# Performance work log

Measured on AMD Instinct MI355X. Metric: run time of the kernel, lower is better.

The kernel has to match this reference:

```python
import jax, jax.numpy as jnp
import numpy as np

B, T, D, H, C = 128, 1000, 40, 128, 8  # batch, time, input feats, hidden, classes


def _lstm_layer(x, Wih, Whh, bih, bhh):
    """Unidirectional LSTM over time. x: [B,T,Din] -> [B,T,H]. PyTorch gate order i,f,g,o."""
    Bn = x.shape[0]
    Hn = Whh.shape[1]
    b = bih + bhh
    def step(carry, xt):
        h, c = carry
        g = xt @ Wih.T + h @ Whh.T + b  # [B,4H]
        i, f, gg, o = jnp.split(g, 4, axis=-1)
        c = jax.nn.sigmoid(f) * c + jax.nn.sigmoid(i) * jnp.tanh(gg)
        h = jax.nn.sigmoid(o) * jnp.tanh(c)
        return (h, c), h
    h0 = jnp.zeros((Bn, Hn), x.dtype)
    _, hs = jax.lax.scan(step, (h0, h0), jnp.swapaxes(x, 0, 1))  # scan over time
    return jnp.swapaxes(hs, 0, 1)


def _bilstm_layer(x, pf, pb):
    fwd = _lstm_layer(x, *pf)
    bwd = jnp.flip(_lstm_layer(jnp.flip(x, 1), *pb), 1)
    return jnp.concatenate([fwd, bwd], axis=-1)  # [B,T,2H]


def setup_inputs() -> dict:
    key = jax.random.key(0)
    ks = jax.random.split(key, 16)
    s = 0.05
    def rn(k, shape):
        return jax.random.normal(k, shape, jnp.float32) * s
    inp = {"x": jax.random.normal(ks[0], (B, T, D), jnp.float32)}
    inp["ln_g"] = jnp.ones((D,), jnp.float32)
    inp["ln_b"] = jnp.zeros((D,), jnp.float32)
    dims = [D, 2 * H]  # layer-0 input feats, layer-1 input feats
    i = 1
    for l in range(2):
        for d in ("f", "b"):
            inp[f"Wih_{d}{l}"] = rn(ks[i], (4 * H, dims[l])); i += 1
            inp[f"Whh_{d}{l}"] = rn(ks[i], (4 * H, H)); i += 1
            inp[f"bih_{d}{l}"] = jnp.zeros((4 * H,), jnp.float32)
            inp[f"bhh_{d}{l}"] = jnp.zeros((4 * H,), jnp.float32)
    inp["attn_W1"] = rn(ks[i], (H, 2 * H)); i += 1
    inp["attn_b1"] = jnp.zeros((H,), jnp.float32)
    inp["attn_w2"] = rn(ks[i], (1, H)); i += 1
    inp["fc_W1"] = rn(ks[i], (H, 2 * H)); i += 1
    inp["fc_b1"] = jnp.zeros((H,), jnp.float32)
    inp["fc_W2"] = rn(ks[i], (C, H)); i += 1
    inp["fc_b2"] = jnp.zeros((C,), jnp.float32)
    return inp


def reference(x, ln_g, ln_b,
              Wih_f0, Whh_f0, bih_f0, bhh_f0, Wih_b0, Whh_b0, bih_b0, bhh_b0,
              Wih_f1, Whh_f1, bih_f1, bhh_f1, Wih_b1, Whh_b1, bih_b1, bhh_b1,
              attn_W1, attn_b1, attn_w2, fc_W1, fc_b1, fc_W2, fc_b2):
    # LayerNorm over feature dim (eps=1e-5, PyTorch default)
    mu = jnp.mean(x, axis=-1, keepdims=True)
    var = jnp.var(x, axis=-1, keepdims=True)
    xn = (x - mu) * jax.lax.rsqrt(var + 1e-5) * ln_g + ln_b
    # 2-layer bidirectional LSTM
    h = _bilstm_layer(xn, (Wih_f0, Whh_f0, bih_f0, bhh_f0), (Wih_b0, Whh_b0, bih_b0, bhh_b0))
    h = _bilstm_layer(h, (Wih_f1, Whh_f1, bih_f1, bhh_f1), (Wih_b1, Whh_b1, bih_b1, bhh_b1))
    # attention pooling: Linear-Tanh-Linear(no bias) -> softmax over time
    scores = jnp.tanh(h @ attn_W1.T + attn_b1) @ attn_w2[0]  # [B,T]
    w = jax.nn.softmax(scores, axis=1)
    ctx = jnp.einsum('bt,btd->bd', w, h)  # [B,2H]
    # MLP classifier head
    hid = jax.nn.relu(ctx @ fc_W1.T + fc_b1)
    return hid @ fc_W2.T + fc_b2  # [B,C] logits
```

## Files before the change

### kernel.cpp

```cpp
#include <hip/hip_runtime.h>

#define T_ 1000

__device__ __forceinline__ float sigf(float x) { return 1.0f / (1.0f + __expf(-x)); }
__device__ __forceinline__ float tanh_fast(float x) { return 1.0f - 2.0f / (1.0f + __expf(2.0f * x)); }
__device__ __forceinline__ float dot4(float4 a, float4 b) {
  return a.x * b.x + a.y * b.y + a.z * b.z + a.w * b.w;
}
__device__ __forceinline__ unsigned short f2bf(float f) {
  unsigned u = __float_as_uint(f);
  u = (u + 0x7fffu + ((u >> 16) & 1u)) >> 16;
  return (unsigned short)u;
}
__device__ __forceinline__ float bf2f(unsigned short h) {
  return __uint_as_float(((unsigned)h) << 16);
}
__device__ __forceinline__ float4 bf4_to_f4(ushort4 u) {
  float4 r;
  r.x = bf2f(u.x); r.y = bf2f(u.y); r.z = bf2f(u.z); r.w = bf2f(u.w);
  return r;
}

__global__ void bail_kernel(float* out, int n) {
  for (int i = threadIdx.x; i < n; i += 256) out[i] = 0.0f;
}

__global__ __launch_bounds__(256) void ln_stats_kernel(const float* __restrict__ x,
                                                       float* __restrict__ mu_arr,
                                                       float* __restrict__ rs_arr) {
  const int lane = threadIdx.x & 63;
  const int w = threadIdx.x >> 6;
  const long row = (long)blockIdx.x * 4 + w;
  float v = (lane < 40) ? x[row * 40 + lane] : 0.0f;
  float s1 = v, s2 = v * v;
  for (int m = 32; m; m >>= 1) {
    s1 += __shfl_xor(s1, m, 64);
    s2 += __shfl_xor(s2, m, 64);
  }
  if (lane == 0) {
    const float mu = s1 * (1.0f / 40.0f);
    const float var = s2 * (1.0f / 40.0f) - mu * mu;
    mu_arr[row] = mu;
    rs_arr[row] = rsqrtf(var + 1e-5f);
  }
}

__global__ __launch_bounds__(512, 1) void rec0_kernel(
    const float* __restrict__ x,
    const float* __restrict__ mu_arr, const float* __restrict__ rs_arr,
    const float* __restrict__ ln_g, const float* __restrict__ ln_b,
    const float* __restrict__ Wih_f, const float* __restrict__ Whh_f,
    const float* __restrict__ bih_f, const float* __restrict__ bhh_f,
    const float* __restrict__ Wih_b, const float* __restrict__ Whh_b,
    const float* __restrict__ bih_b, const float* __restrict__ bhh_b,
    float* __restrict__ h0) {
  const int tid = threadIdx.x;
  const int u = (tid >> 6) * 16 + ((tid & 63) >> 2);
  const int p = tid & 3;
  const int brow = blockIdx.x & 127;
  const int dir = blockIdx.x >> 7;
  const float* __restrict__ Wih = dir ? Wih_b : Wih_f;
  const float* __restrict__ Whh = dir ? Whh_b : Whh_f;
  const float* __restrict__ bih = dir ? bih_b : bih_f;
  const float* __restrict__ bhh = dir ? bhh_b : bhh_f;

  float4 wh[4][8];
  float4 wi[4][3];
  float S1[4], bias[4];
#pragma unroll
  for (int g = 0; g < 4; ++g) {
    const int row = g * 128 + u;
    const float4* wr = (const float4*)(Whh + row * 128 + p * 32);
#pragma unroll
    for (int ff = 0; ff < 8; ++ff) wh[g][ff] = wr[(ff + 2 * p) & 7];
    float s1p = 0.0f, s2p = 0.0f;
#pragma unroll
    for (int f = 0; f < 3; ++f) {
      float tmp[4];
#pragma unroll
      for (int e = 0; e < 4; ++e) {
        const int k = p * 12 + f * 4 + e;
        const float wv = (k < 40) ? Wih[row * 40 + k] : 0.0f;
        const float gk = (k < 40) ? ln_g[k] : 0.0f;
        const float bk = (k < 40) ? ln_b[k] : 0.0f;
        const float wf = wv * gk;
        tmp[e] = wf;
        s1p += wf;
        s2p += wv * bk;
      }
      wi[g][f] = make_float4(tmp[0], tmp[1], tmp[2], tmp[3]);
    }
    s1p += __shfl_xor(s1p, 1, 64); s1p += __shfl_xor(s1p, 2, 64);
    s2p += __shfl_xor(s2p, 1, 64); s2p += __shfl_xor(s2p, 2, 64);
    S1[g] = s1p;
    bias[g] = bih[g * 128 + u] + bhh[g * 128 + u] + s2p;
  }

  __shared__ float h4f[128];
  __shared__ __align__(16) float x_ring[2][8][48];
  __shared__ float mu_ring[2][8], rs_ring[2][8];
  __shared__ float hring[2][8][128];

  const int lr8 = tid / 40;
  const int lcol = tid - lr8 * 40;
  const long xbase = (long)brow * T_ * 40;
  const long mbase = (long)brow * T_;
  const long hbase = (long)brow * T_ * 256;

  if (tid < 128) h4f[tid] = 0.0f;
  if (tid < 128) {
    const int b = tid >> 6, r = (tid >> 3) & 7, cc = 40 + (tid & 7);
    x_ring[b][r][cc] = 0.0f;
  }
  if (tid < 320) {
    const int t = lr8;
    const int tt = dir ? (T_ - 1 - t) : t;
    x_ring[0][lr8][lcol] = x[xbase + (long)tt * 40 + lcol];
  } else if (tid < 328) {
    const int t = tid - 320;
    const int tt = dir ? (T_ - 1 - t) : t;
    mu_ring[0][t] = mu_arr[mbase + tt];
  } else if (tid < 336) {
    const int t = tid - 328;
    const int tt = dir ? (T_ - 1 - t) : t;
    rs_ring[0][t] = rs_arr[mbase + tt];
  }
  float c = 0.0f;
  float xpf = 0.0f, mupf = 0.0f, rspf = 0.0f;
  __syncthreads();

  for (int sb = 0; sb < 125; ++sb) {
    const int rb = sb & 1;
#pragma unroll
    for (int su = 0; su < 8; ++su) {
      if (su == 0) {
        if (sb + 1 < 125) {
          if (tid < 320) {
            const int t = (sb + 1) * 8 + lr8;
            const int tt = dir ? (T_ - 1 - t) : t;
            xpf = x[xbase + (long)tt * 40 + lcol];
          } else if (tid < 328) {
            const int t = (sb + 1) * 8 + (tid - 320);
            const int tt = dir ? (T_ - 1 - t) : t;
            mupf = mu_arr[mbase + tt];
          } else if (tid < 336) {
            const int t = (sb + 1) * 8 + (tid - 328);
            const int tt = dir ? (T_ - 1 - t) : t;
            rspf = rs_arr[mbase + tt];
          }
        }
        if (sb > 0) {
#pragma unroll
          for (int e = 0; e < 2; ++e) {
            const int idx = tid + e * 512;
            const int v = idx >> 7, j = idx & 127;
            const int ts = (sb - 1) * 8 + v;
            const int te = dir ? (T_ - 1 - ts) : ts;
            h0[hbase + (long)te * 256 + dir * 128 + j] = hring[rb ^ 1][v][j];
          }
        }
      }
      float a0 = 0.f, a1 = 0.f, a2 = 0.f, a3 = 0.f;
      const float4* h4v = (const float4*)h4f;
#pragma unroll
      for (int ff = 0; ff < 8; ++ff) {
        const float4 hv = h4v[p * 8 + ((ff + 2 * p) & 7)];
        a0 += dot4(hv, wh[0][ff]);
        a1 += dot4(hv, wh[1][ff]);
        a2 += dot4(hv, wh[2][ff]);
        a3 += dot4(hv, wh[3][ff]);
      }
      float x0 = 0.f, x1 = 0.f, x2 = 0.f, x3 = 0.f;
      const float4* xr4 = (const float4*)x_ring[rb][su];
#pragma unroll
      for (int f = 0; f < 3; ++f) {
        const float4 xv = xr4[p * 3 + f];
        x0 += dot4(xv, wi[0][f]);
        x1 += dot4(xv, wi[1][f]);
        x2 += dot4(xv, wi[2][f]);
        x3 += dot4(xv, wi[3][f]);
      }
      const float rs = rs_ring[rb][su];
      const float mu = mu_ring[rb][su];
      float pg[4];
      pg[0] = a0 + rs * x0;
      pg[1] = a1 + rs * x1;
      pg[2] = a2 + rs * x2;
      pg[3] = a3 + rs * x3;
#pragma unroll
      for (int g = 0; g < 4; ++g) {
        pg[g] += __shfl_xor(pg[g], 1, 64);
        pg[g] += __shfl_xor(pg[g], 2, 64);
        pg[g] += bias[g] - rs * mu * S1[g];
      }
      const float ig = sigf(pg[0]);
      const float fg = sigf(pg[1]);
      const float gg = tanh_fast(pg[2]);
      const float og = sigf(pg[3]);
      c = fg * c + ig * gg;
      const float hv = og * tanh_fast(c);
      if (p == 0) { h4f[u] = hv; hring[rb][su][u] = hv; }
      if (su == 7 && sb + 1 < 125) {
        if (tid < 320) x_ring[rb ^ 1][lr8][lcol] = xpf;
        else if (tid < 328) mu_ring[rb ^ 1][tid - 320] = mupf;
        else if (tid < 336) rs_ring[rb ^ 1][tid - 328] = rspf;
      }
      __syncthreads();
    }
  }
#pragma unroll
  for (int e = 0; e < 2; ++e) {
    const int idx = tid + e * 512;
    const int v = idx >> 7, j = idx & 127;
    const int ts = 124 * 8 + v;
    const int te = dir ? (T_ - 1 - ts) : ts;
    h0[hbase + (long)te * 256 + dir * 128 + j] = hring[0][v][j];
  }
}

__global__ __launch_bounds__(512, 1) void rec1_kernel(
    const float* __restrict__ xw_f, const float* __restrict__ xw_b,
    const float* __restrict__ Whh_f, const float* __restrict__ bih_f, const float* __restrict__ bhh_f,
    const float* __restrict__ Whh_b, const float* __restrict__ bih_b, const float* __restrict__ bhh_b,
    unsigned short* __restrict__ h1b, float* __restrict__ state,
    int Tc, int t0f, int t0b, int first) {
  const int tid = threadIdx.x;
  const int u = (tid >> 6) * 16 + ((tid & 63) >> 2);
  const int p = tid & 3;
  const int brow = blockIdx.x & 127;
  const int dir = blockIdx.x >> 7;
  const float* __restrict__ xw = dir ? xw_b : xw_f;
  const float* __restrict__ Whh = dir ? Whh_b : Whh_f;
  const float* __restrict__ bih = dir ? bih_b : bih_f;
  const float* __restrict__ bhh = dir ? bhh_b : bhh_f;
  const int t0 = dir ? t0b : t0f;

  float4 wh[4][8];
#pragma unroll
  for (int g = 0; g < 4; ++g) {
    const float4* wr = (const float4*)(Whh + (g * 128 + u) * 128 + p * 32);
#pragma unroll
    for (int ff = 0; ff < 8; ++ff) wh[g][ff] = wr[(ff + 2 * p) & 7];
  }
  const int myrow = p * 128 + u;
  const float bias_p = bih[myrow] + bhh[myrow];

  __shared__ float h4f[128];
  __shared__ float hring[2][8][128];
  float* sblk = state + (long)blockIdx.x * 256;
  float c = 0.0f;
  if (first) {
    if (tid < 128) h4f[tid] = 0.0f;
  } else {
    if (tid < 128) h4f[tid] = sblk[tid];
    c = sblk[128 + u];
  }
  const long gbase = (long)brow * Tc;
  float xr[8];
#pragma unroll
  for (int v = 0; v < 8; ++v) {
    xr[v] = 0.0f;
    if (v < Tc) {
      const int tr = dir ? (Tc - 1 - v) : v;
      xr[v] = xw[(gbase + tr) * 512 + myrow];
    }
  }
  __syncthreads();

  const int nSB = (Tc + 7) / 8;
  for (int sb = 0; sb < nSB; ++sb) {
    const int rb = sb & 1;
#pragma unroll
    for (int su = 0; su < 8; ++su) {
      const int s = sb * 8 + su;
      if (s >= Tc) break;
      if (su == 0 && sb > 0) {
#pragma unroll
        for (int e = 0; e < 2; ++e) {
          const int idx = tid + e * 512;
          const int v = idx >> 7, j = idx & 127;
          const int s2 = (sb - 1) * 8 + v;
          const int tt = dir ? (Tc - 1 - s2) : s2;
          h1b[((long)brow * T_ + (t0 + tt)) * 256 + dir * 128 + j] = f2bf(hring[rb ^ 1][v][j]);
        }
      }
      float a0 = 0.f, a1 = 0.f, a2 = 0.f, a3 = 0.f;
      const float4* h4v = (const float4*)h4f;
#pragma unroll
      for (int ff = 0; ff < 8; ++ff) {
        const float4 hv = h4v[p * 8 + ((ff + 2 * p) & 7)];
        a0 += dot4(hv, wh[0][ff]);
        a1 += dot4(hv, wh[1][ff]);
        a2 += dot4(hv, wh[2][ff]);
        a3 += dot4(hv, wh[3][ff]);
      }
      const float xin = xr[su] + bias_p;
      float pg[4];
      pg[0] = a0 + ((p == 0) ? xin : 0.0f);
      pg[1] = a1 + ((p == 1) ? xin : 0.0f);
      pg[2] = a2 + ((p == 2) ? xin : 0.0f);
      pg[3] = a3 + ((p == 3) ? xin : 0.0f);
#pragma unroll
      for (int g = 0; g < 4; ++g) {
        pg[g] += __shfl_xor(pg[g], 1, 64);
        pg[g] += __shfl_xor(pg[g], 2, 64);
      }
      const float ig = sigf(pg[0]);
      const float fg = sigf(pg[1]);
      const float gg = tanh_fast(pg[2]);
      const float og = sigf(pg[3]);
      c = fg * c + ig * gg;
      const float hv = og * tanh_fast(c);
      if (p == 0) { h4f[u] = hv; hring[rb][su][u] = hv; }
      if (su == 7) {
#pragma unroll
        for (int v = 0; v < 8; ++v) {
          const int sn = s + 1 + v;
          xr[v] = 0.0f;
          if (sn < Tc) {
            const int tr = dir ? (Tc - 1 - sn) : sn;
            xr[v] = xw[(gbase + tr) * 512 + myrow];
          }
        }
      }
      __syncthreads();
    }
  }
  {
    const int sbL = (Tc - 1) >> 3;
    const int cnt = Tc - sbL * 8;
    const int rbL = sbL & 1;
#pragma unroll
    for (int e = 0; e < 2; ++e) {
      const int idx = tid + e * 512;
      const int v = idx >> 7, j = idx & 127;
      if (v < cnt) {
        const int s2 = sbL * 8 + v;
        const int tt = dir ? (Tc - 1 - s2) : s2;
        h1b[((long)brow * T_ + (t0 + tt)) * 256 + dir * 128 + j] = f2bf(hring[rbL][v][j]);
      }
    }
  }
  if (tid < 128) sblk[tid] = h4f[tid];
  if (p == 0) sblk[128 + u] = c;
}

__global__ __launch_bounds__(256, 2) void gemm_xw1(
    const float* __restrict__ h0,
    const float* __restrict__ Wf, const float* __restrict__ Wb,
    float* __restrict__ xwf, float* __restrict__ xwb,
    int Tc, int t0f, int t0b) {
  __shared__ float As[64 * 36];
  __shared__ float Bs[128 * 36];
  __shared__ int rowbase[64];
  const int tid = threadIdx.x;
  const int tx = tid & 15, ty = tid >> 4;
  const int r0 = blockIdx.x * 64;
  const int jt = blockIdx.y;
  const int dir = jt >> 2;
  const int nh = jt & 3;
  const float* __restrict__ W = dir ? Wb : Wf;
  float* __restrict__ out = dir ? xwb : xwf;
  const int jbase = nh * 128;
  const int t0 = dir ? t0b : t0f;

  if (tid < 64) {
    const int r = r0 + tid;
    const int br = r / Tc;
    rowbase[tid] = br * T_ + t0 + (r - br * Tc);
  }

  float4* As4 = (float4*)As;
  float4* Bs4 = (float4*)Bs;
  float acc[4][8] = {};
#pragma unroll 1
  for (int kk = 0; kk < 8; ++kk) {
    __syncthreads();
#pragma unroll
    for (int i = 0; i < 2; ++i) {
      const int q = tid + i * 256;
      const int row = q >> 3, k4 = q & 7;
      As4[row * 9 + k4] = *(const float4*)&h0[(long)rowbase[row] * 256 + kk * 32 + k4 * 4];
    }
#pragma unroll
    for (int i = 0; i < 4; ++i) {
      const int q = tid + i * 256;
      const int row = q >> 3, k4 = q & 7;
      Bs4[row * 9 + k4] = *(const float4*)&W[(long)(jbase + row) * 256 + kk * 32 + k4 * 4];
    }
    __syncthreads();
#pragma unroll 1
    for (int k4 = 0; k4 < 8; ++k4) {
      float4 av[4];
#pragma unroll
      for (int r = 0; r < 4; ++r) av[r] = As4[(ty * 4 + r) * 9 + k4];
#pragma unroll
      for (int c2 = 0; c2 < 8; ++c2) {
        const float4 bv = Bs4[(tx + 16 * c2) * 9 + k4];
#pragma unroll
        for (int r = 0; r < 4; ++r) acc[r][c2] += dot4(av[r], bv);
      }
    }
  }
#pragma unroll
  for (int r = 0; r < 4; ++r) {
    const long ob = (long)(r0 + ty * 4 + r) * 512 + jbase + tx;
#pragma unroll
    for (int c2 = 0; c2 < 8; ++c2) out[ob + c2 * 16] = acc[r][c2];
  }
}

__global__ __launch_bounds__(256, 2) void score_kernel(
    const unsigned short* __restrict__ h1b, const float* __restrict__ W1,
    const float* __restrict__ b1, const float* __restrict__ w2,
    float* __restrict__ scores) {
  __shared__ float As[64 * 36];
  __shared__ float Bs[128 * 36];
  const int tid = threadIdx.x;
  const int tx = tid & 15, ty = tid >> 4;
  const long r0 = (long)blockIdx.x * 64;

  float4* As4 = (float4*)As;
  float4* Bs4 = (float4*)Bs;
  float acc[4][8] = {};
#pragma unroll 1
  for (int kk = 0; kk < 8; ++kk) {
    __syncthreads();
#pragma unroll
    for (int i = 0; i < 2; ++i) {
      const int q = tid + i * 256;
      const int row = q >> 3, k4 = q & 7;
      const ushort4 uv = *(const ushort4*)&h1b[(r0 + row) * 256 + kk * 32 + k4 * 4];
      As4[row * 9 + k4] = bf4_to_f4(uv);
    }
#pragma unroll
    for (int i = 0; i < 4; ++i) {
      const int q = tid + i * 256;
      const int row = q >> 3, k4 = q & 7;
      Bs4[row * 9 + k4] = *(const float4*)&W1[(long)row * 256 + kk * 32 + k4 * 4];
    }
    __syncthreads();
#pragma unroll 1
    for (int k4 = 0; k4 < 8; ++k4) {
      float4 av[4];
#pragma unroll
      for (int r = 0; r < 4; ++r) av[r] = As4[(ty * 4 + r) * 9 + k4];
#pragma unroll
      for (int c2 = 0; c2 < 8; ++c2) {
        const float4 bv = Bs4[(tx + 16 * c2) * 9 + k4];
#pragma unroll
        for (int r = 0; r < 4; ++r) acc[r][c2] += dot4(av[r], bv);
      }
    }
  }
#pragma unroll
  for (int r = 0; r < 4; ++r) {
    float s = 0.0f;
#pragma unroll
    for (int c2 = 0; c2 < 8; ++c2) {
      const int col = tx + 16 * c2;
      s += tanh_fast(acc[r][c2] + b1[col]) * w2[col];
    }
#pragma unroll
    for (int m = 1; m < 16; m <<= 1) s += __shfl_xor(s, m, 16);
    if (tx == 0) scores[r0 + ty * 4 + r] = s;
  }
}

__global__ __launch_bounds__(256, 2) void head_kernel(
    const float* __restrict__ scores, const unsigned short* __restrict__ h1b,
    const float* __restrict__ fW1, const float* __restrict__ fb1,
    const float* __restrict__ fW2, const float* __restrict__ fb2,
    float* __restrict__ outp) {
  const int b = blockIdx.x, tid = threadIdx.x;
  __shared__ float wls[1000];
  __shared__ float red[8];
  __shared__ __align__(16) float ctx[256];
  __shared__ __align__(16) float hid[128];

  float sv[4];
  float mx = -1e30f;
#pragma unroll
  for (int i = 0; i < 4; ++i) {
    const int t = tid + i * 256;
    sv[i] = (t < 1000) ? scores[b * 1000 + t] : -1e30f;
    mx = fmaxf(mx, sv[i]);
  }
  for (int m = 32; m; m >>= 1) mx = fmaxf(mx, __shfl_xor(mx, m, 64));
  if ((tid & 63) == 0) red[tid >> 6] = mx;
  __syncthreads();
  mx = fmaxf(fmaxf(red[0], red[1]), fmaxf(red[2], red[3]));
  float se = 0.0f;
#pragma unroll
  for (int i = 0; i < 4; ++i) {
    const int t = tid + i * 256;
    if (t < 1000) {
      const float e = __expf(sv[i] - mx);
      wls[t] = e;
      se += e;
    }
  }
  for (int m = 32; m; m >>= 1) se += __shfl_xor(se, m, 64);
  if ((tid & 63) == 0) red[4 + (tid >> 6)] = se;
  __syncthreads();
  const float rinv = 1.0f / (red[4] + red[5] + red[6] + red[7]);

  float a = 0.0f;
  const unsigned short* hb = h1b + (long)b * T_ * 256 + tid;
  for (int t = 0; t < T_; ++t) a = fmaf(wls[t], bf2f(hb[t * 256]), a);
  ctx[tid] = a * rinv;
  __syncthreads();
  if (tid < 128) {
    float s = fb1[tid];
    const float4* wr = (const float4*)&fW1[tid * 256];
    const float4* cc = (const float4*)ctx;
#pragma unroll
    for (int f = 0; f < 64; ++f) s += dot4(wr[f], cc[f]);
    hid[tid] = fmaxf(s, 0.0f);
  }
  __syncthreads();
  if (tid < 8) {
    float s = fb2[tid];
    const float4* wr = (const float4*)&fW2[tid * 128];
    const float4* hh = (const float4*)hid;
#pragma unroll
    for (int f = 0; f < 32; ++f) s += dot4(wr[f], hh[f]);
    outp[b * 8 + tid] = s;
  }
}

extern "C" void kernel_launch(void* const* d_in, const int* in_sizes, int n_in,
                              void* d_out, int out_size, void* d_ws, size_t ws_size,
                              hipStream_t stream) {
  (void)in_sizes; (void)n_in; (void)out_size;
  const float* x       = (const float*)d_in[0];
  const float* ln_g    = (const float*)d_in[1];
  const float* ln_b    = (const float*)d_in[2];
  const float* Wih_f0  = (const float*)d_in[3];
  const float* Whh_f0  = (const float*)d_in[4];
  const float* bih_f0  = (const float*)d_in[5];
  const float* bhh_f0  = (const float*)d_in[6];
  const float* Wih_b0  = (const float*)d_in[7];
  const float* Whh_b0  = (const float*)d_in[8];
  const float* bih_b0  = (const float*)d_in[9];
  const float* bhh_b0  = (const float*)d_in[10];
  const float* Wih_f1  = (const float*)d_in[11];
  const float* Whh_f1  = (const float*)d_in[12];
  const float* bih_f1  = (const float*)d_in[13];
  const float* bhh_f1  = (const float*)d_in[14];
  const float* Wih_b1  = (const float*)d_in[15];
  const float* Whh_b1  = (const float*)d_in[16];
  const float* bih_b1  = (const float*)d_in[17];
  const float* bhh_b1  = (const float*)d_in[18];
  const float* attn_W1 = (const float*)d_in[19];
  const float* attn_b1 = (const float*)d_in[20];
  const float* attn_w2 = (const float*)d_in[21];
  const float* fc_W1   = (const float*)d_in[22];
  const float* fc_b1   = (const float*)d_in[23];
  const float* fc_W2   = (const float*)d_in[24];
  const float* fc_b2   = (const float*)d_in[25];

  char* base = (char*)d_ws;
  size_t off = 0;
  auto alloc = [&](size_t bytes) {
    char* ptr = base + off;
    off += (bytes + 255) & ~(size_t)255;
    return ptr;
  };
  float*          h0    = (float*)alloc(32768000ull * 4);
  unsigned short* h1b   = (unsigned short*)alloc(32768000ull * 2);
  float*          state = (float*)alloc(65536ull * 4);
  float*          scor  = (float*)alloc(128000ull * 4);
  float*          mu_a  = (float*)alloc(128000ull * 4);
  float*          rs_a  = (float*)alloc(128000ull * 4);

  const size_t rem = (ws_size > off) ? (ws_size - off) : 0;
  static const int cands[16] = {1000, 500, 250, 200, 125, 100, 50, 40, 25, 20, 10, 8, 5, 4, 2, 1};
  int Tc = 0;
  for (int ci = 0; ci < 16; ++ci) {
    if (524288ull * (size_t)cands[ci] <= rem) { Tc = cands[ci]; break; }
  }
  if (Tc == 0) {
    bail_kernel<<<dim3(1), dim3(256), 0, stream>>>((float*)d_out, 1024);
    return;
  }
  float* xwf = (float*)(base + off);
  float* xwb = xwf + 65536L * Tc;

  ln_stats_kernel<<<dim3(32000), dim3(256), 0, stream>>>(x, mu_a, rs_a);
  rec0_kernel<<<dim3(256), dim3(512), 0, stream>>>(x, mu_a, rs_a, ln_g, ln_b,
                                                   Wih_f0, Whh_f0, bih_f0, bhh_f0,
                                                   Wih_b0, Whh_b0, bih_b0, bhh_b0, h0);
  const int nch = T_ / Tc;
  for (int ch = 0; ch < nch; ++ch) {
    const int t0f = ch * Tc;
    const int t0b = T_ - (ch + 1) * Tc;
    gemm_xw1<<<dim3(2 * Tc, 8), dim3(256), 0, stream>>>(h0, Wih_f1, Wih_b1, xwf, xwb, Tc, t0f, t0b);
    rec1_kernel<<<dim3(256), dim3(512), 0, stream>>>(xwf, xwb, Whh_f1, bih_f1, bhh_f1,
                                                     Whh_b1, bih_b1, bhh_b1, h1b, state,
                                                     Tc, t0f, t0b, (ch == 0) ? 1 : 0);
  }
  score_kernel<<<dim3(2000), dim3(256), 0, stream>>>(h1b, attn_W1, attn_b1, attn_w2, scor);
  head_kernel<<<dim3(128), dim3(256), 0, stream>>>(scor, h1b, fc_W1, fc_b1, fc_W2, fc_b2,
                                                   (float*)d_out);
}
```

Measured before the change: 3.569 ms.

## Split LSTM recurrence across 8 lanes per unit with 1024-thread blocks and double-buffered h

Both recurrent kernels now use 1024 threads per block, with 8 lanes cooperating on each hidden unit instead of 4. This halves the per-thread Whh dot-product length and the register footprint, at the cost of one extra shuffle-reduction stage per step. The shared hidden-state vector is double-buffered (read one copy, write the other) so a step's write cannot race with reads of the previous h. The aim is to shorten the serial critical path per timestep through more parallelism, while adding more waves per barrier and more reduction latency.

```diff
diff --git a/kernel.cpp b/kernel.cpp
--- a/kernel.cpp
+++ b/kernel.cpp
@@ -45,7 +45,7 @@
   }
 }
 
-__global__ __launch_bounds__(512, 1) void rec0_kernel(
+__global__ __launch_bounds__(1024, 1) void rec0_kernel(
     const float* __restrict__ x,
     const float* __restrict__ mu_arr, const float* __restrict__ rs_arr,
     const float* __restrict__ ln_g, const float* __restrict__ ln_b,
@@ -55,8 +55,8 @@
     const float* __restrict__ bih_b, const float* __restrict__ bhh_b,
     float* __restrict__ h0) {
   const int tid = threadIdx.x;
-  const int u = (tid >> 6) * 16 + ((tid & 63) >> 2);
-  const int p = tid & 3;
+  const int u = (tid >> 6) * 8 + ((tid & 63) >> 3);
+  const int p = tid & 7;
   const int brow = blockIdx.x & 127;
   const int dir = blockIdx.x >> 7;
   const float* __restrict__ Wih = dir ? Wih_b : Wih_f;
@@ -64,22 +64,22 @@
   const float* __restrict__ bih = dir ? bih_b : bih_f;
   const float* __restrict__ bhh = dir ? bhh_b : bhh_f;
 
-  float4 wh[4][8];
-  float4 wi[4][3];
+  float4 wh[4][4];
+  float2 wi[4][3];
   float S1[4], bias[4];
 #pragma unroll
   for (int g = 0; g < 4; ++g) {
     const int row = g * 128 + u;
-    const float4* wr = (const float4*)(Whh + row * 128 + p * 32);
-#pragma unroll
-    for (int ff = 0; ff < 8; ++ff) wh[g][ff] = wr[(ff + 2 * p) & 7];
+    const float4* wr4 = (const float4*)(Whh + row * 128 + p * 16);
+#pragma unroll
+    for (int ff = 0; ff < 4; ++ff) wh[g][ff] = wr4[(ff + p) & 3];
     float s1p = 0.0f, s2p = 0.0f;
 #pragma unroll
     for (int f = 0; f < 3; ++f) {
-      float tmp[4];
-#pragma unroll
-      for (int e = 0; e < 4; ++e) {
-        const int k = p * 12 + f * 4 + e;
+      float tmp[2];
+#pragma unroll
+      for (int e = 0; e < 2; ++e) {
+        const int k = p * 6 + f * 2 + e;
         const float wv = (k < 40) ? Wih[row * 40 + k] : 0.0f;
         const float gk = (k < 40) ? ln_g[k] : 0.0f;
         const float bk = (k < 40) ? ln_b[k] : 0.0f;
@@ -88,15 +88,15 @@
         s1p += wf;
         s2p += wv * bk;
       }
-      wi[g][f] = make_float4(tmp[0], tmp[1], tmp[2], tmp[3]);
-    }
-    s1p += __shfl_xor(s1p, 1, 64); s1p += __shfl_xor(s1p, 2, 64);
-    s2p += __shfl_xor(s2p, 1, 64); s2p += __shfl_xor(s2p, 2, 64);
+      wi[g][f] = make_float2(tmp[0], tmp[1]);
+    }
+    s1p += __shfl_xor(s1p, 1, 64); s1p += __shfl_xor(s1p, 2, 64); s1p += __shfl_xor(s1p, 4, 64);
+    s2p += __shfl_xor(s2p, 1, 64); s2p += __shfl_xor(s2p, 2, 64); s2p += __shfl_xor(s2p, 4, 64);
     S1[g] = s1p;
     bias[g] = bih[g * 128 + u] + bhh[g * 128 + u] + s2p;
   }
 
-  __shared__ float h4f[128];
+  __shared__ float h4f[2][128];
   __shared__ __align__(16) float x_ring[2][8][48];
   __shared__ float mu_ring[2][8], rs_ring[2][8];
   __shared__ float hring[2][8][128];
@@ -107,7 +107,7 @@
   const long mbase = (long)brow * T_;
   const long hbase = (long)brow * T_ * 256;
 
-  if (tid < 128) h4f[tid] = 0.0f;
+  if (tid < 128) h4f[0][tid] = 0.0f;
   if (tid < 128) {
     const int b = tid >> 6, r = (tid >> 3) & 7, cc = 40 + (tid & 7);
     x_ring[b][r][cc] = 0.0f;
@@ -133,6 +133,7 @@
     const int rb = sb & 1;
 #pragma unroll
     for (int su = 0; su < 8; ++su) {
+      const int rdq = su & 1, wrq = rdq ^ 1;
       if (su == 0) {
         if (sb + 1 < 125) {
           if (tid < 320) {
@@ -150,35 +151,31 @@
           }
         }
         if (sb > 0) {
-#pragma unroll
-          for (int e = 0; e < 2; ++e) {
-            const int idx = tid + e * 512;
-            const int v = idx >> 7, j = idx & 127;
-            const int ts = (sb - 1) * 8 + v;
-            const int te = dir ? (T_ - 1 - ts) : ts;
-            h0[hbase + (long)te * 256 + dir * 128 + j] = hring[rb ^ 1][v][j];
-          }
+          const int v = tid >> 7, j = tid & 127;
+          const int ts = (sb - 1) * 8 + v;
+          const int te = dir ? (T_ - 1 - ts) : ts;
+          h0[hbase + (long)te * 256 + dir * 128 + j] = hring[rb ^ 1][v][j];
         }
       }
       float a0 = 0.f, a1 = 0.f, a2 = 0.f, a3 = 0.f;
-      const float4* h4v = (const float4*)h4f;
-#pragma unroll
-      for (int ff = 0; ff < 8; ++ff) {
-        const float4 hv = h4v[p * 8 + ((ff + 2 * p) & 7)];
+      const float4* h4v = (const float4*)h4f[rdq];
+#pragma unroll
+      for (int ff = 0; ff < 4; ++ff) {
+        const float4 hv = h4v[p * 4 + ((ff + p) & 3)];
         a0 += dot4(hv, wh[0][ff]);
         a1 += dot4(hv, wh[1][ff]);
         a2 += dot4(hv, wh[2][ff]);
         a3 += dot4(hv, wh[3][ff]);
       }
       float x0 = 0.f, x1 = 0.f, x2 = 0.f, x3 = 0.f;
-      const float4* xr4 = (const float4*)x_ring[rb][su];
+      const float2* xr2 = (const float2*)&x_ring[rb][su][p * 6];
 #pragma unroll
       for (int f = 0; f < 3; ++f) {
-        const float4 xv = xr4[p * 3 + f];
-        x0 += dot4(xv, wi[0][f]);
-        x1 += dot4(xv, wi[1][f]);
-        x2 += dot4(xv, wi[2][f]);
-        x3 += dot4(xv, wi[3][f]);
+        const float2 xv = xr2[f];
+        x0 += wi[0][f].x * xv.x + wi[0][f].y * xv.y;
+        x1 += wi[1][f].x * xv.x + wi[1][f].y * xv.y;
+        x2 += wi[2][f].x * xv.x + wi[2][f].y * xv.y;
+        x3 += wi[3][f].x * xv.x + wi[3][f].y * xv.y;
       }
       const float rs = rs_ring[rb][su];
       const float mu = mu_ring[rb][su];
@@ -191,6 +188,7 @@
       for (int g = 0; g < 4; ++g) {
         pg[g] += __shfl_xor(pg[g], 1, 64);
         pg[g] += __shfl_xor(pg[g], 2, 64);
+        pg[g] += __shfl_xor(pg[g], 4, 64);
         pg[g] += bias[g] - rs * mu * S1[g];
       }
       const float ig = sigf(pg[0]);
@@ -199,7 +197,7 @@
       const float og = sigf(pg[3]);
       c = fg * c + ig * gg;
       const float hv = og * tanh_fast(c);
-      if (p == 0) { h4f[u] = hv; hring[rb][su][u] = hv; }
+      if (p == 0) { h4f[wrq][u] = hv; hring[rb][su][u] = hv; }
       if (su == 7 && sb + 1 < 125) {
         if (tid < 320) x_ring[rb ^ 1][lr8][lcol] = xpf;
         else if (tid < 328) mu_ring[rb ^ 1][tid - 320] = mupf;
@@ -208,25 +206,23 @@
       __syncthreads();
     }
   }
-#pragma unroll
-  for (int e = 0; e < 2; ++e) {
-    const int idx = tid + e * 512;
-    const int v = idx >> 7, j = idx & 127;
+  {
+    const int v = tid >> 7, j = tid & 127;
     const int ts = 124 * 8 + v;
     const int te = dir ? (T_ - 1 - ts) : ts;
     h0[hbase + (long)te * 256 + dir * 128 + j] = hring[0][v][j];
   }
 }
 
-__global__ __launch_bounds__(512, 1) void rec1_kernel(
+__global__ __launch_bounds__(1024, 1) void rec1_kernel(
     const float* __restrict__ xw_f, const float* __restrict__ xw_b,
     const float* __restrict__ Whh_f, const float* __restrict__ bih_f, const float* __restrict__ bhh_f,
     const float* __restrict__ Whh_b, const float* __restrict__ bih_b, const float* __restrict__ bhh_b,
     unsigned short* __restrict__ h1b, float* __restrict__ state,
     int Tc, int t0f, int t0b, int first) {
   const int tid = threadIdx.x;
-  const int u = (tid >> 6) * 16 + ((tid & 63) >> 2);
-  const int p = tid & 3;
+  const int u = (tid >> 6) * 8 + ((tid & 63) >> 3);
+  const int p = tid & 7;
   const int brow = blockIdx.x & 127;
   const int dir = blockIdx.x >> 7;
   const float* __restrict__ xw = dir ? xw_b : xw_f;
@@ -235,24 +231,24 @@
   const float* __restrict__ bhh = dir ? bhh_b : bhh_f;
   const int t0 = dir ? t0b : t0f;
 
-  float4 wh[4][8];
+  float4 wh[4][4];
 #pragma unroll
   for (int g = 0; g < 4; ++g) {
-    const float4* wr = (const float4*)(Whh + (g * 128 + u) * 128 + p * 32);
-#pragma unroll
-    for (int ff = 0; ff < 8; ++ff) wh[g][ff] = wr[(ff + 2 * p) & 7];
+    const float4* wr4 = (const float4*)(Whh + (g * 128 + u) * 128 + p * 16);
+#pragma unroll
+    for (int ff = 0; ff < 4; ++ff) wh[g][ff] = wr4[(ff + p) & 3];
   }
   const int myrow = p * 128 + u;
-  const float bias_p = bih[myrow] + bhh[myrow];
-
-  __shared__ float h4f[128];
+  const float bias_p = (p < 4) ? (bih[myrow] + bhh[myrow]) : 0.0f;
+
+  __shared__ float h4f[2][128];
   __shared__ float hring[2][8][128];
   float* sblk = state + (long)blockIdx.x * 256;
   float c = 0.0f;
   if (first) {
-    if (tid < 128) h4f[tid] = 0.0f;
+    if (tid < 128) h4f[0][tid] = 0.0f;
   } else {
-    if (tid < 128) h4f[tid] = sblk[tid];
+    if (tid < 128) h4f[0][tid] = sblk[tid];
     c = sblk[128 + u];
   }
   const long gbase = (long)brow * Tc;
@@ -260,7 +256,7 @@
 #pragma unroll
   for (int v = 0; v < 8; ++v) {
     xr[v] = 0.0f;
-    if (v < Tc) {
+    if (p < 4 && v < Tc) {
       const int tr = dir ? (Tc - 1 - v) : v;
       xr[v] = xw[(gbase + tr) * 512 + myrow];
     }
@@ -274,21 +270,18 @@
     for (int su = 0; su < 8; ++su) {
       const int s = sb * 8 + su;
       if (s >= Tc) break;
+      const int rdq = su & 1, wrq = rdq ^ 1;
       if (su == 0 && sb > 0) {
-#pragma unroll
-        for (int e = 0; e < 2; ++e) {
-          const int idx = tid + e * 512;
-          const int v = idx >> 7, j = idx & 127;
-          const int s2 = (sb - 1) * 8 + v;
-          const int tt = dir ? (Tc - 1 - s2) : s2;
-          h1b[((long)brow * T_ + (t0 + tt)) * 256 + dir * 128 + j] = f2bf(hring[rb ^ 1][v][j]);
-        }
+        const int v = tid >> 7, j = tid & 127;
+        const int s2 = (sb - 1) * 8 + v;
+        const int tt = dir ? (Tc - 1 - s2) : s2;
+        h1b[((long)brow * T_ + (t0 + tt)) * 256 + dir * 128 + j] = f2bf(hring[rb ^ 1][v][j]);
       }
       float a0 = 0.f, a1 = 0.f, a2 = 0.f, a3 = 0.f;
-      const float4* h4v = (const float4*)h4f;
-#pragma unroll
-      for (int ff = 0; ff < 8; ++ff) {
-        const float4 hv = h4v[p * 8 + ((ff + 2 * p) & 7)];
+      const float4* h4v = (const float4*)h4f[rdq];
+#pragma unroll
+      for (int ff = 0; ff < 4; ++ff) {
+        const float4 hv = h4v[p * 4 + ((ff + p) & 3)];
         a0 += dot4(hv, wh[0][ff]);
         a1 += dot4(hv, wh[1][ff]);
         a2 += dot4(hv, wh[2][ff]);
@@ -304,6 +297,7 @@
       for (int g = 0; g < 4; ++g) {
         pg[g] += __shfl_xor(pg[g], 1, 64);
         pg[g] += __shfl_xor(pg[g], 2, 64);
+        pg[g] += __shfl_xor(pg[g], 4, 64);
       }
       const float ig = sigf(pg[0]);
       const float fg = sigf(pg[1]);
@@ -311,13 +305,13 @@
       const float og = sigf(pg[3]);
       c = fg * c + ig * gg;
       const float hv = og * tanh_fast(c);
-      if (p == 0) { h4f[u] = hv; hring[rb][su][u] = hv; }
+      if (p == 0) { h4f[wrq][u] = hv; hring[rb][su][u] = hv; }
       if (su == 7) {
 #pragma unroll
         for (int v = 0; v < 8; ++v) {
           const int sn = s + 1 + v;
           xr[v] = 0.0f;
-          if (sn < Tc) {
+          if (p < 4 && sn < Tc) {
             const int tr = dir ? (Tc - 1 - sn) : sn;
             xr[v] = xw[(gbase + tr) * 512 + myrow];
           }
@@ -330,18 +324,14 @@
     const int sbL = (Tc - 1) >> 3;
     const int cnt = Tc - sbL * 8;
     const int rbL = sbL & 1;
-#pragma unroll
-    for (int e = 0; e < 2; ++e) {
-      const int idx = tid + e * 512;
-      const int v = idx >> 7, j = idx & 127;
-      if (v < cnt) {
-        const int s2 = sbL * 8 + v;
-        const int tt = dir ? (Tc - 1 - s2) : s2;
-        h1b[((long)brow * T_ + (t0 + tt)) * 256 + dir * 128 + j] = f2bf(hring[rbL][v][j]);
-      }
-    }
-  }
-  if (tid < 128) sblk[tid] = h4f[tid];
+    const int v = tid >> 7, j = tid & 127;
+    if (v < cnt) {
+      const int s2 = sbL * 8 + v;
+      const int tt = dir ? (Tc - 1 - s2) : s2;
+      h1b[((long)brow * T_ + (t0 + tt)) * 256 + dir * 128 + j] = f2bf(hring[rbL][v][j]);
+    }
+  }
+  if (tid < 128) sblk[tid] = h4f[Tc & 1][tid];
   if (p == 0) sblk[128 + u] = c;
 }
 
@@ -588,17 +578,17 @@
   float* xwb = xwf + 65536L * Tc;
 
   ln_stats_kernel<<<dim3(32000), dim3(256), 0, stream>>>(x, mu_a, rs_a);
-  rec0_kernel<<<dim3(256), dim3(512), 0, stream>>>(x, mu_a, rs_a, ln_g, ln_b,
-                                                   Wih_f0, Whh_f0, bih_f0, bhh_f0,
-                                                   Wih_b0, Whh_b0, bih_b0, bhh_b0, h0);
+  rec0_kernel<<<dim3(256), dim3(1024), 0, stream>>>(x, mu_a, rs_a, ln_g, ln_b,
+                                                    Wih_f0, Whh_f0, bih_f0, bhh_f0,
+                                                    Wih_b0, Whh_b0, bih_b0, bhh_b0, h0);
   const int nch = T_ / Tc;
   for (int ch = 0; ch < nch; ++ch) {
     const int t0f = ch * Tc;
     const int t0b = T_ - (ch + 1) * Tc;
     gemm_xw1<<<dim3(2 * Tc, 8), dim3(256), 0, stream>>>(h0, Wih_f1, Wih_b1, xwf, xwb, Tc, t0f, t0b);
-    rec1_kernel<<<dim3(256), dim3(512), 0, stream>>>(xwf, xwb, Whh_f1, bih_f1, bhh_f1,
-                                                     Whh_b1, bih_b1, bhh_b1, h1b, state,
-                                                     Tc, t0f, t0b, (ch == 0) ? 1 : 0);
+    rec1_kernel<<<dim3(256), dim3(1024), 0, stream>>>(xwf, xwb, Whh_f1, bih_f1, bhh_f1,
+                                                      Whh_b1, bih_b1, bhh_b1, h1b, state,
+                                                      Tc, t0f, t0b, (ch == 0) ? 1 : 0);
   }
   score_kernel<<<dim3(2000), dim3(256), 0, stream>>>(h1b, attn_W1, attn_b1, attn_w2, scor);
   head_kernel<<<dim3(128), dim3(256), 0, stream>>>(scor, h1b, fc_W1, fc_b1, fc_W2, fc_b2,
```

Result: slower. 4.292 ms (+20.3%).
